# Kernel tuning notes

Measured on AMD Instinct MI355X. Metric: run time of the kernel, lower is better.

## Reference

```python
import jax, jax.numpy as jnp
import numpy as np

NCLS, NDF, B = 256, 512, 1024
ALP = 0.1


def setup_inputs() -> dict:
    key = jax.random.key(0)
    k1, k2, k3 = jax.random.split(key, 3)
    df = jax.random.normal(k1, (B, NDF), dtype=jnp.float32)
    gt = jax.random.randint(k2, (B,), 0, NCLS)
    fc = jax.random.normal(k3, (NCLS, NDF), dtype=jnp.float32)
    return {"df": df, "gt": gt, "fc": fc}


def _update_stats(df, gt):
    """Sequential per-sample running mean/var update (moving_avg=False branch).
    Faithful to the torch no_grad loop: per-class counter `it`, c1=it/(it+1),
    c2=1/(it+1); mean[t]=f when it==0 else mean[t]*c1+f*c2;
    var[t]=var[t]*c1 + (f-mean[t])**2 * c1*c2. Buffers start at zero.
    """
    mean0 = jnp.zeros((NCLS, NDF), jnp.float32)
    var0 = jnp.zeros((NCLS, NDF), jnp.float32)
    it0 = jnp.zeros((NCLS,), jnp.int32)

    def step(carry, xt):
        mean, var, it = carry
        f, t = xt
        n = it[t]
        nf = n.astype(jnp.float32)
        c1 = nf / (nf + 1.0)
        c2 = 1.0 / (nf + 1.0)
        m_t = jnp.where(n == 0, f, mean[t] * c1 + f * c2)
        a = (f - m_t) ** 2
        v_t = var[t] * c1 + a * c1 * c2
        return (mean.at[t].set(m_t), var.at[t].set(v_t), it.at[t].add(1)), None

    (mean, var, it), _ = jax.lax.scan(step, (mean0, var0, it0), (df, gt))
    return mean, var


def reference(df, gt, fc):
    # stats updated from detached features (torch uses no_grad)
    _, var = _update_stats(jax.lax.stop_gradient(df), gt)
    Var = var[gt]          # (B, ndf)
    Fc = fc[gt]            # (B, ndf): column of fc for each sample's class
    W = fc[None, :, :] - Fc[:, None, :]  # (B, ncls, ndf)
    # score[b,c] = W[b,c,:].df[b,:] + alp/2 * (W**2)[b,c,:].Var[b,:]
    score = jnp.einsum('bcd,bd->bc', W, df) \
        + 0.5 * ALP * jnp.einsum('bcd,bd->bc', W * W, Var)
    return score[:, :, None]  # (B, ncls, 1), matching torch matmul output
```

## Files before the change

### kernel.cpp

```cpp
#include <hip/hip_runtime.h>

#define NCLS 256
#define NDF  512
#define BSZ  1024
#define ALP  0.1f


typedef __attribute__((ext_vector_type(8))) short bf16x8;
typedef __attribute__((ext_vector_type(4))) float f32x4;

__device__ __forceinline__ unsigned rne_pk(float lo, float hi) {
    union { float f; unsigned u; } a, b;
    a.f = lo; b.f = hi;
    unsigned ua = (a.u + 0x7FFFu + ((a.u >> 16) & 1u)) >> 16;
    unsigned ub = (b.u + 0x7FFFu + ((b.u >> 16) & 1u)) & 0xFFFF0000u;
    return ua | ub;
}
__device__ __forceinline__ uint4 pk16(float4 p, float4 q) {
    uint4 r;
    r.x = rne_pk(p.x, p.y); r.y = rne_pk(p.z, p.w);
    r.z = rne_pk(q.x, q.y); r.w = rne_pk(q.z, q.w);
    return r;
}

__global__ __launch_bounds__(256) void fused_main(const float* __restrict__ df,
                                                  const int* __restrict__ gt,
                                                  const float* __restrict__ fc,
                                                  float* __restrict__ s1p,
                                                  float* __restrict__ Rp) {
    __shared__ alignas(16) char Asb[64 * 128];
    __shared__ alignas(16) char Bsb[64 * 128];
    __shared__ int gts[BSZ];
    __shared__ unsigned long long bmap[64 * 16];

    const int tid = threadIdx.x;
    const int bid = blockIdx.x;
    const int lane = tid & 63;
    const int wv = tid >> 6;
    const int wm = (wv >> 1) * 32, wn = (wv & 1) * 32;
    const int fr = lane & 15;
    const int fkb = (lane >> 4) * 16;
    const int fswz = (fr & 7) << 4;

    const int sr = tid >> 2;
    const int skb = (tid & 3) * 32;
    const int sswz = (sr & 7) << 4;
    char* arow = Asb + sr * 128;
    char* brow = Bsb + sr * 128;

    f32x4 acc[2][2];
    acc[0][0] = 0.f; acc[0][1] = 0.f; acc[1][0] = 0.f; acc[1][1] = 0.f;

    auto mma_step = [&](int k0b) {
        const int kb = (k0b + fkb) ^ fswz;
        const bf16x8 aF0 = *(const bf16x8*)(Asb + (wm + fr) * 128 + kb);
        const bf16x8 aF1 = *(const bf16x8*)(Asb + (wm + 16 + fr) * 128 + kb);
        const bf16x8 bF0 = *(const bf16x8*)(Bsb + (wn + fr) * 128 + kb);
        const bf16x8 bF1 = *(const bf16x8*)(Bsb + (wn + 16 + fr) * 128 + kb);
        acc[0][0] = __builtin_amdgcn_mfma_f32_16x16x32_bf16(aF0, bF0, acc[0][0], 0, 0, 0);
        acc[0][1] = __builtin_amdgcn_mfma_f32_16x16x32_bf16(aF0, bF1, acc[0][1], 0, 0, 0);
        acc[1][0] = __builtin_amdgcn_mfma_f32_16x16x32_bf16(aF1, bF0, acc[1][0], 0, 0, 0);
        acc[1][1] = __builtin_amdgcn_mfma_f32_16x16x32_bf16(aF1, bF1, acc[1][1], 0, 0, 0);
    };
    auto store_tile = [&](float* base) {
#pragma unroll
        for (int mi = 0; mi < 2; ++mi)
#pragma unroll
            for (int ni = 0; ni < 2; ++ni)
#pragma unroll
                for (int r2 = 0; r2 < 4; ++r2)
                    base[(wm + mi * 16 + (lane >> 4) * 4 + r2) * NCLS + wn + ni * 16 + fr] =
                        acc[mi][ni][r2];
    };

    if (bid < 256) {
        const int z = bid & 3;
        const int tile = bid >> 2;
        const int bm = tile & 15, bn = tile >> 4;
        const float* Ag = df + (bm * 64 + sr) * NDF + z * 128 + (tid & 3) * 16;
        const float* Bg = fc + (bn * 64 + sr) * NDF + z * 128 + (tid & 3) * 16;

        float4 a0 = ((const float4*)Ag)[0], a1 = ((const float4*)Ag)[1],
               a2 = ((const float4*)Ag)[2], a3 = ((const float4*)Ag)[3];
        float4 b0 = ((const float4*)Bg)[0], b1 = ((const float4*)Bg)[1],
               b2 = ((const float4*)Bg)[2], b3 = ((const float4*)Bg)[3];
        *(uint4*)(arow + (skb ^ sswz)) = pk16(a0, a1);
        *(uint4*)(arow + ((skb + 16) ^ sswz)) = pk16(a2, a3);
        *(uint4*)(brow + (skb ^ sswz)) = pk16(b0, b1);
        *(uint4*)(brow + ((skb + 16) ^ sswz)) = pk16(b2, b3);
        __syncthreads();
        a0 = ((const float4*)(Ag + 64))[0]; a1 = ((const float4*)(Ag + 64))[1];
        a2 = ((const float4*)(Ag + 64))[2]; a3 = ((const float4*)(Ag + 64))[3];
        b0 = ((const float4*)(Bg + 64))[0]; b1 = ((const float4*)(Bg + 64))[1];
        b2 = ((const float4*)(Bg + 64))[2]; b3 = ((const float4*)(Bg + 64))[3];
        mma_step(0); mma_step(64);
        __syncthreads();
        *(uint4*)(arow + (skb ^ sswz)) = pk16(a0, a1);
        *(uint4*)(arow + ((skb + 16) ^ sswz)) = pk16(a2, a3);
        *(uint4*)(brow + (skb ^ sswz)) = pk16(b0, b1);
        *(uint4*)(brow + ((skb + 16) ^ sswz)) = pk16(b2, b3);
        __syncthreads();
        mma_step(0); mma_step(64);
        store_tile(s1p + z * (BSZ * NCLS) + (bm * 64) * NCLS + bn * 64);
    } else {
        const int r = bid - 256;
        const int z = r & 7;
        const int tile = r >> 3;
        const int bm = tile & 3, bn = tile >> 2;
        const int D0 = z * 64;
        const int clocal = sr;
        const int dg = tid & 3;
        const int myclass = bm * 64 + clocal;
        const int dim0 = D0 + dg * 16;

        const float* Bg = fc + (bn * 64 + sr) * NDF + D0 + (tid & 3) * 16;
        const float4 b0 = ((const float4*)Bg)[0], b1 = ((const float4*)Bg)[1],
                     b2 = ((const float4*)Bg)[2], b3 = ((const float4*)Bg)[3];

        for (int i = tid; i < BSZ; i += 256) gts[i] = gt[i];
        for (int i = tid; i < 1024; i += 256) bmap[i] = 0ull;
        __syncthreads();
        for (int i = tid; i < BSZ; i += 256) {
            const int c = gts[i] - bm * 64;
            if ((unsigned)c < 64u) atomicOr(&bmap[c * 16 + (i >> 6)], 1ull << (i & 63));
        }
        const float* fct = fc + myclass * NDF + dim0;
        float fcq[16];
        {
            const float4 q0 = ((const float4*)fct)[0], q1 = ((const float4*)fct)[1];
            const float4 q2 = ((const float4*)fct)[2], q3 = ((const float4*)fct)[3];
            fcq[0]=q0.x; fcq[1]=q0.y; fcq[2]=q0.z; fcq[3]=q0.w;
            fcq[4]=q1.x; fcq[5]=q1.y; fcq[6]=q1.z; fcq[7]=q1.w;
            fcq[8]=q2.x; fcq[9]=q2.y; fcq[10]=q2.z; fcq[11]=q2.w;
            fcq[12]=q3.x; fcq[13]=q3.y; fcq[14]=q3.z; fcq[15]=q3.w;
        }
        __syncthreads();

        float m[16], v[16];
#pragma unroll
        for (int j = 0; j < 16; ++j) { m[j] = 0.f; v[j] = 0.f; }
        float nf = 0.f;
        {
            int w = 0;
            unsigned long long bits = bmap[clocal * 16];
            auto next = [&]() -> int {
                while (bits == 0ull) {
                    if (w >= 15) return -1;
                    bits = bmap[clocal * 16 + (++w)];
                }
                const int b = __ffsll((unsigned long long)bits) - 1;
                bits &= bits - 1ull;
                return (w << 6) + b;
            };
            int cur = next();
            float f[16];
            if (cur >= 0) {
                const float* p = df + cur * NDF + dim0;
                const float4 q0 = ((const float4*)p)[0], q1 = ((const float4*)p)[1];
                const float4 q2 = ((const float4*)p)[2], q3 = ((const float4*)p)[3];
                f[0]=q0.x; f[1]=q0.y; f[2]=q0.z; f[3]=q0.w;
                f[4]=q1.x; f[5]=q1.y; f[6]=q1.z; f[7]=q1.w;
                f[8]=q2.x; f[9]=q2.y; f[10]=q2.z; f[11]=q2.w;
                f[12]=q3.x; f[13]=q3.y; f[14]=q3.z; f[15]=q3.w;
            }
            while (cur >= 0) {
                const int nxt = next();
                float g[16];
                if (nxt >= 0) {
                    const float* p = df + nxt * NDF + dim0;
                    const float4 q0 = ((const float4*)p)[0], q1 = ((const float4*)p)[1];
                    const float4 q2 = ((const float4*)p)[2], q3 = ((const float4*)p)[3];
                    g[0]=q0.x; g[1]=q0.y; g[2]=q0.z; g[3]=q0.w;
                    g[4]=q1.x; g[5]=q1.y; g[6]=q1.z; g[7]=q1.w;
                    g[8]=q2.x; g[9]=q2.y; g[10]=q2.z; g[11]=q2.w;
                    g[12]=q3.x; g[13]=q3.y; g[14]=q3.z; g[15]=q3.w;
                }
                const float c2 = 1.0f / (nf + 1.0f);
                const float c1 = nf * c2;
                const float c12 = c1 * c2;
#pragma unroll
                for (int j = 0; j < 16; ++j) {
                    m[j] = m[j] * c1 + f[j] * c2;
                    const float a = f[j] - m[j];
                    v[j] = v[j] * c1 + a * a * c12;
                }
                nf += 1.0f;
#pragma unroll
                for (int j = 0; j < 16; ++j) f[j] = g[j];
                cur = nxt;
            }
        }

        {
            float4 p0, p1, p2, p3;
            p0.x=-2.f*fcq[0]*v[0];  p0.y=-2.f*fcq[1]*v[1];  p0.z=-2.f*fcq[2]*v[2];  p0.w=-2.f*fcq[3]*v[3];
            p1.x=-2.f*fcq[4]*v[4];  p1.y=-2.f*fcq[5]*v[5];  p1.z=-2.f*fcq[6]*v[6];  p1.w=-2.f*fcq[7]*v[7];
            p2.x=-2.f*fcq[8]*v[8];  p2.y=-2.f*fcq[9]*v[9];  p2.z=-2.f*fcq[10]*v[10]; p2.w=-2.f*fcq[11]*v[11];
            p3.x=-2.f*fcq[12]*v[12]; p3.y=-2.f*fcq[13]*v[13]; p3.z=-2.f*fcq[14]*v[14]; p3.w=-2.f*fcq[15]*v[15];
            *(uint4*)(arow + (skb ^ sswz)) = pk16(p0, p1);
            *(uint4*)(arow + ((skb + 16) ^ sswz)) = pk16(p2, p3);
            *(uint4*)(brow + (skb ^ sswz)) = pk16(b0, b1);
            *(uint4*)(brow + ((skb + 16) ^ sswz)) = pk16(b2, b3);
        }
        __syncthreads();
        mma_step(0); mma_step(64);
        __syncthreads();
        {
            float4 p0, p1, p2, p3, s0, s1, s2, s3;
            p0.x=v[0];  p0.y=v[1];  p0.z=v[2];  p0.w=v[3];
            p1.x=v[4];  p1.y=v[5];  p1.z=v[6];  p1.w=v[7];
            p2.x=v[8];  p2.y=v[9];  p2.z=v[10]; p2.w=v[11];
            p3.x=v[12]; p3.y=v[13]; p3.z=v[14]; p3.w=v[15];
            s0.x=b0.x*b0.x; s0.y=b0.y*b0.y; s0.z=b0.z*b0.z; s0.w=b0.w*b0.w;
            s1.x=b1.x*b1.x; s1.y=b1.y*b1.y; s1.z=b1.z*b1.z; s1.w=b1.w*b1.w;
            s2.x=b2.x*b2.x; s2.y=b2.y*b2.y; s2.z=b2.z*b2.z; s2.w=b2.w*b2.w;
            s3.x=b3.x*b3.x; s3.y=b3.y*b3.y; s3.z=b3.z*b3.z; s3.w=b3.w*b3.w;
            *(uint4*)(arow + (skb ^ sswz)) = pk16(p0, p1);
            *(uint4*)(arow + ((skb + 16) ^ sswz)) = pk16(p2, p3);
            *(uint4*)(brow + (skb ^ sswz)) = pk16(s0, s1);
            *(uint4*)(brow + ((skb + 16) ^ sswz)) = pk16(s2, s3);
        }
        __syncthreads();
        mma_step(0); mma_step(64);
        store_tile(Rp + z * (NCLS * NCLS) + (bm * 64) * NCLS + bn * 64);
    }
}

__global__ __launch_bounds__(256) void epilogue_kernel(const float* __restrict__ s1p,
                                                       const float* __restrict__ Rp,
                                                       const int* __restrict__ gt,
                                                       float* __restrict__ out) {
    const int b = blockIdx.x * 4 + (threadIdx.x >> 6);
    const int cq = (threadIdx.x & 63) * 4;
    const int t = gt[b];
    float4 v1 = make_float4(0.f, 0.f, 0.f, 0.f);
    float v1t = 0.f;
#pragma unroll
    for (int zz = 0; zz < 4; ++zz) {
        const float* row = s1p + zz * (BSZ * NCLS) + b * NCLS;
        const float4 q = *(const float4*)(row + cq);
        v1.x += q.x; v1.y += q.y; v1.z += q.z; v1.w += q.w;
        v1t += row[t];
    }
    float4 vR = make_float4(0.f, 0.f, 0.f, 0.f);
    float vRt = 0.f;
#pragma unroll
    for (int zz = 0; zz < 8; ++zz) {
        const float* row = Rp + zz * (NCLS * NCLS) + t * NCLS;
        const float4 q = *(const float4*)(row + cq);
        vR.x += q.x; vR.y += q.y; vR.z += q.z; vR.w += q.w;
        vRt += row[t];
    }
    float4 o;
    o.x = (v1.x - v1t) + 0.5f * ALP * (vR.x - vRt);
    o.y = (v1.y - v1t) + 0.5f * ALP * (vR.y - vRt);
    o.z = (v1.z - v1t) + 0.5f * ALP * (vR.z - vRt);
    o.w = (v1.w - v1t) + 0.5f * ALP * (vR.w - vRt);
    *(float4*)(out + b * NCLS + cq) = o;
}

extern "C" void kernel_launch(void* const* d_in, const int* in_sizes, int n_in,
                              void* d_out, int out_size, void* d_ws, size_t ws_size,
                              hipStream_t stream) {
    const float* df = (const float*)d_in[0];
    const int* gt = (const int*)d_in[1];
    const float* fc = (const float*)d_in[2];
    float* out = (float*)d_out;

    float* ws = (float*)d_ws;
    float* s1p = ws;
    float* Rp = s1p + 4 * BSZ * NCLS;

    fused_main<<<384, 256, 0, stream>>>(df, gt, fc, s1p, Rp);
    epilogue_kernel<<<256, 256, 0, stream>>>(s1p, Rp, gt, out);
}
```

Measured before the change: 25.10 us.

## Split GEMM K dimension 8-way, reorder stats blocks first, union shared memory

```diff
diff --git a/kernel.cpp b/kernel.cpp
--- a/kernel.cpp
+++ b/kernel.cpp
@@ -28,10 +28,10 @@
                                                   const float* __restrict__ fc,
                                                   float* __restrict__ s1p,
                                                   float* __restrict__ Rp) {
-    __shared__ alignas(16) char Asb[64 * 128];
-    __shared__ alignas(16) char Bsb[64 * 128];
-    __shared__ int gts[BSZ];
-    __shared__ unsigned long long bmap[64 * 16];
+    __shared__ union {
+        struct { alignas(16) char A[64 * 128]; alignas(16) char B[64 * 128]; } g;
+        struct { int gts[BSZ]; unsigned long long bmap[64 * 16]; } r;
+    } sm;
 
     const int tid = threadIdx.x;
     const int bid = blockIdx.x;
@@ -45,18 +45,16 @@
     const int sr = tid >> 2;
     const int skb = (tid & 3) * 32;
     const int sswz = (sr & 7) << 4;
-    char* arow = Asb + sr * 128;
-    char* brow = Bsb + sr * 128;
 
     f32x4 acc[2][2];
     acc[0][0] = 0.f; acc[0][1] = 0.f; acc[1][0] = 0.f; acc[1][1] = 0.f;
 
     auto mma_step = [&](int k0b) {
         const int kb = (k0b + fkb) ^ fswz;
-        const bf16x8 aF0 = *(const bf16x8*)(Asb + (wm + fr) * 128 + kb);
-        const bf16x8 aF1 = *(const bf16x8*)(Asb + (wm + 16 + fr) * 128 + kb);
-        const bf16x8 bF0 = *(const bf16x8*)(Bsb + (wn + fr) * 128 + kb);
-        const bf16x8 bF1 = *(const bf16x8*)(Bsb + (wn + 16 + fr) * 128 + kb);
+        const bf16x8 aF0 = *(const bf16x8*)(sm.g.A + (wm + fr) * 128 + kb);
+        const bf16x8 aF1 = *(const bf16x8*)(sm.g.A + (wm + 16 + fr) * 128 + kb);
+        const bf16x8 bF0 = *(const bf16x8*)(sm.g.B + (wn + fr) * 128 + kb);
+        const bf16x8 bF1 = *(const bf16x8*)(sm.g.B + (wn + 16 + fr) * 128 + kb);
         acc[0][0] = __builtin_amdgcn_mfma_f32_16x16x32_bf16(aF0, bF0, acc[0][0], 0, 0, 0);
         acc[0][1] = __builtin_amdgcn_mfma_f32_16x16x32_bf16(aF0, bF1, acc[0][1], 0, 0, 0);
         acc[1][0] = __builtin_amdgcn_mfma_f32_16x16x32_bf16(aF1, bF0, acc[1][0], 0, 0, 0);
@@ -73,39 +71,31 @@
                         acc[mi][ni][r2];
     };
 
-    if (bid < 256) {
-        const int z = bid & 3;
-        const int tile = bid >> 2;
+    char* arow = sm.g.A + sr * 128;
+    char* brow = sm.g.B + sr * 128;
+
+    if (bid >= 128) {
+        const int sid = bid - 128;
+        const int z = sid & 7;
+        const int tile = sid >> 3;
         const int bm = tile & 15, bn = tile >> 4;
-        const float* Ag = df + (bm * 64 + sr) * NDF + z * 128 + (tid & 3) * 16;
-        const float* Bg = fc + (bn * 64 + sr) * NDF + z * 128 + (tid & 3) * 16;
-
-        float4 a0 = ((const float4*)Ag)[0], a1 = ((const float4*)Ag)[1],
-               a2 = ((const float4*)Ag)[2], a3 = ((const float4*)Ag)[3];
-        float4 b0 = ((const float4*)Bg)[0], b1 = ((const float4*)Bg)[1],
-               b2 = ((const float4*)Bg)[2], b3 = ((const float4*)Bg)[3];
+        const float* Ag = df + (bm * 64 + sr) * NDF + z * 64 + (tid & 3) * 16;
+        const float* Bg = fc + (bn * 64 + sr) * NDF + z * 64 + (tid & 3) * 16;
+
+        const float4 a0 = ((const float4*)Ag)[0], a1 = ((const float4*)Ag)[1],
+                     a2 = ((const float4*)Ag)[2], a3 = ((const float4*)Ag)[3];
+        const float4 b0 = ((const float4*)Bg)[0], b1 = ((const float4*)Bg)[1],
+                     b2 = ((const float4*)Bg)[2], b3 = ((const float4*)Bg)[3];
         *(uint4*)(arow + (skb ^ sswz)) = pk16(a0, a1);
         *(uint4*)(arow + ((skb + 16) ^ sswz)) = pk16(a2, a3);
         *(uint4*)(brow + (skb ^ sswz)) = pk16(b0, b1);
         *(uint4*)(brow + ((skb + 16) ^ sswz)) = pk16(b2, b3);
         __syncthreads();
-        a0 = ((const float4*)(Ag + 64))[0]; a1 = ((const float4*)(Ag + 64))[1];
-        a2 = ((const float4*)(Ag + 64))[2]; a3 = ((const float4*)(Ag + 64))[3];
-        b0 = ((const float4*)(Bg + 64))[0]; b1 = ((const float4*)(Bg + 64))[1];
-        b2 = ((const float4*)(Bg + 64))[2]; b3 = ((const float4*)(Bg + 64))[3];
-        mma_step(0); mma_step(64);
-        __syncthreads();
-        *(uint4*)(arow + (skb ^ sswz)) = pk16(a0, a1);
-        *(uint4*)(arow + ((skb + 16) ^ sswz)) = pk16(a2, a3);
-        *(uint4*)(brow + (skb ^ sswz)) = pk16(b0, b1);
-        *(uint4*)(brow + ((skb + 16) ^ sswz)) = pk16(b2, b3);
-        __syncthreads();
         mma_step(0); mma_step(64);
         store_tile(s1p + z * (BSZ * NCLS) + (bm * 64) * NCLS + bn * 64);
     } else {
-        const int r = bid - 256;
-        const int z = r & 7;
-        const int tile = r >> 3;
+        const int z = bid & 7;
+        const int tile = bid >> 3;
         const int bm = tile & 3, bn = tile >> 2;
         const int D0 = z * 64;
         const int clocal = sr;
@@ -117,12 +107,12 @@
         const float4 b0 = ((const float4*)Bg)[0], b1 = ((const float4*)Bg)[1],
                      b2 = ((const float4*)Bg)[2], b3 = ((const float4*)Bg)[3];
 
-        for (int i = tid; i < BSZ; i += 256) gts[i] = gt[i];
-        for (int i = tid; i < 1024; i += 256) bmap[i] = 0ull;
+        for (int i = tid; i < BSZ; i += 256) sm.r.gts[i] = gt[i];
+        for (int i = tid; i < 1024; i += 256) sm.r.bmap[i] = 0ull;
         __syncthreads();
         for (int i = tid; i < BSZ; i += 256) {
-            const int c = gts[i] - bm * 64;
-            if ((unsigned)c < 64u) atomicOr(&bmap[c * 16 + (i >> 6)], 1ull << (i & 63));
+            const int c = sm.r.gts[i] - bm * 64;
+            if ((unsigned)c < 64u) atomicOr(&sm.r.bmap[c * 16 + (i >> 6)], 1ull << (i & 63));
         }
         const float* fct = fc + myclass * NDF + dim0;
         float fcq[16];
@@ -142,11 +132,11 @@
         float nf = 0.f;
         {
             int w = 0;
-            unsigned long long bits = bmap[clocal * 16];
+            unsigned long long bits = sm.r.bmap[clocal * 16];
             auto next = [&]() -> int {
                 while (bits == 0ull) {
                     if (w >= 15) return -1;
-                    bits = bmap[clocal * 16 + (++w)];
+                    bits = sm.r.bmap[clocal * 16 + (++w)];
                 }
                 const int b = __ffsll((unsigned long long)bits) - 1;
                 bits &= bits - 1ull;
@@ -190,6 +180,7 @@
                 cur = nxt;
             }
         }
+        __syncthreads();
 
         {
             float4 p0, p1, p2, p3;
@@ -236,7 +227,7 @@
     float4 v1 = make_float4(0.f, 0.f, 0.f, 0.f);
     float v1t = 0.f;
 #pragma unroll
-    for (int zz = 0; zz < 4; ++zz) {
+    for (int zz = 0; zz < 8; ++zz) {
         const float* row = s1p + zz * (BSZ * NCLS) + b * NCLS;
         const float4 q = *(const float4*)(row + cq);
         v1.x += q.x; v1.y += q.y; v1.z += q.z; v1.w += q.w;
@@ -269,8 +260,8 @@
 
     float* ws = (float*)d_ws;
     float* s1p = ws;
-    float* Rp = s1p + 4 * BSZ * NCLS;
-
-    fused_main<<<384, 256, 0, stream>>>(df, gt, fc, s1p, Rp);
+    float* Rp = s1p + 8 * BSZ * NCLS;
+
+    fused_main<<<640, 256, 0, stream>>>(df, gt, fc, s1p, Rp);
     epilogue_kernel<<<256, 256, 0, stream>>>(s1p, Rp, gt, out);
 }
```

Result: slower. 27.25 us (+8.6%).
